# Performance work log

Hardware: AMD Instinct MI355X
Metric: run time of the kernel (lower is better)

The kernel has to match this reference:

```python
import jax, jax.numpy as jnp
import numpy as np

SL, BS, HS = 2048, 4, 1024
FFN, E, TOPK = 4096, 8, 2
T = SL * BS


def setup_inputs() -> dict:
    key = jax.random.key(0)
    k1, k2, k3, k4, k5 = jax.random.split(key, 5)
    x = jax.random.normal(k1, (SL, BS, HS), dtype=jnp.float32)
    expert_weights = jax.random.uniform(k2, (T, TOPK), dtype=jnp.float32)
    w1 = jax.random.normal(k3, (E, HS, FFN), dtype=jnp.float32) * (HS ** -0.5)
    w2 = jax.random.normal(k4, (E, FFN, HS), dtype=jnp.float32) * (FFN ** -0.5)
    expert_indices = jax.random.randint(k5, (T, TOPK), 0, E, dtype=jnp.int32)
    return {"x": x, "expert_weights": expert_weights, "w1": w1, "w2": w2,
            "expert_indices": expert_indices}


def reference(x, expert_weights, w1, w2, expert_indices):
    """Dropless MoE: dispatch each token to its top_k experts, run the
    per-expert MLP (x @ W1 -> gelu -> @ W2), combine weighted copies.

    Equivalent math to megablocks sort/gather -> grouped GEMM -> scatter:
    each (token, k) row is processed by exactly expert_indices[t, k]'s MLP
    and the results are summed back per token with expert_weights.
    """
    in_shape = x.shape
    hs = x.shape[-1]
    xf = x.reshape(-1, hs)                      # [T, H]
    top_k = expert_indices.shape[-1]
    eids = expert_indices.reshape(-1)           # [T*top_k]
    # gather: replicate each token top_k times (row j <-> token j // top_k)
    x_rep = jnp.repeat(xf, top_k, axis=0)       # [T*top_k, H]

    def per_expert(acc, ewb):
        e, w1_e, w2_e = ewb
        h = jax.nn.gelu(x_rep @ w1_e)           # [T*top_k, F]
        y = h @ w2_e                            # [T*top_k, H]
        mask = (eids == e).astype(x.dtype)[:, None]
        return acc + mask * y, None

    n_exp = w1.shape[0]
    acc0 = jnp.zeros_like(x_rep)
    out_flat, _ = jax.lax.scan(per_expert, acc0, (jnp.arange(n_exp), w1, w2))
    # scatter-combine: weighted sum of the top_k expert outputs per token
    w_flat = expert_weights.reshape(-1, 1)      # [T*top_k, 1]
    out = (w_flat * out_flat).reshape(-1, top_k, hs).sum(axis=1)
    return out.reshape(in_shape)
```

## Files before the change

### kernel.cpp

```cpp
#include <hip/hip_runtime.h>
#include <hip/hip_bf16.h>
#include <stdint.h>
#include <stddef.h>

#define SLEN 2048
#define BSZ  4
#define HSD  1024
#define FFND 4096
#define NEXP 8
#define NTOP 2
#define NTOK (SLEN*BSZ)
#define NROW (NTOK*NTOP)
#define NRP  (NROW + NEXP*128)
#define MAXT (NROW/128 + NEXP)

typedef __hip_bfloat16 bf16;
typedef __attribute__((ext_vector_type(8))) __bf16 b8v;
typedef __attribute__((ext_vector_type(4))) float f4v;

static constexpr size_t OFF_BLOCKHIST = 0;
static constexpr size_t OFF_BLOCKBASE = 2048;
static constexpr size_t OFF_SCHED_E   = 4096;
static constexpr size_t OFF_SCHED_R   = 4736;
static constexpr size_t OFF_NTILES    = 5376;
static constexpr size_t OFF_STOK      = 16384;
static constexpr size_t OFF_SWT       = OFF_STOK + 69632;
static constexpr size_t OFF_SLOT      = OFF_SWT + 69632;
static constexpr size_t OFF_XB        = 221184;
static constexpr size_t OFF_W1T       = OFF_XB  + (size_t)NTOK*HSD*2;
static constexpr size_t OFF_W2T       = OFF_W1T + (size_t)NEXP*FFND*HSD*2;
static constexpr size_t OFF_H         = OFF_W2T + (size_t)NEXP*HSD*FFND*2;
static constexpr size_t OFF_Y         = OFF_H   + (size_t)NRP*FFND*2;
static constexpr size_t WS_NEED       = OFF_Y   + (size_t)NRP*HSD*2;
static constexpr size_t OFF_YP        = OFF_XB;

__device__ __forceinline__ void gload_lds16(const void* g, void* l) {
  __builtin_amdgcn_global_load_lds(
      (const __attribute__((address_space(1))) unsigned int*)g,
      (__attribute__((address_space(3))) unsigned int*)l, 16, 0, 0);
}

__device__ __forceinline__ f4v mfma16(b8v a, b8v b, f4v c) {
  return __builtin_amdgcn_mfma_f32_16x16x32_bf16(a, b, c, 0, 0, 0);
}

__device__ __forceinline__ float gelu_tanh(float x) {
  float u = 0.7978845608028654f * x * (1.0f + 0.044715f * x * x);
  float e = __expf(2.0f * u);
  float t = 1.0f - 2.0f / (e + 1.0f);
  return 0.5f * x * (1.0f + t);
}

__global__ void moe_hist(const int* __restrict__ eidx, int* __restrict__ blockhist) {
  __shared__ int h[NEXP];
  int tid = threadIdx.x;
  if (tid < NEXP) h[tid] = 0;
  __syncthreads();
  int gid = blockIdx.x * 256 + tid;
  atomicAdd(&h[eidx[gid] & 7], 1);
  __syncthreads();
  if (tid < NEXP) blockhist[blockIdx.x * NEXP + tid] = h[tid];
}

__global__ void moe_plan(const int* __restrict__ blockhist, int* __restrict__ blockbase,
                         int* __restrict__ sched_e, int* __restrict__ sched_r,
                         int* __restrict__ ntiles,
                         int* __restrict__ stok, float* __restrict__ swt) {
  int tid = threadIdx.x;
  for (int i = tid; i < NRP; i += 256) { stok[i] = 0; swt[i] = 0.0f; }
  __syncthreads();
  if (tid == 0) {
    int cnt[NEXP], off[NEXP];
    for (int e = 0; e < NEXP; ++e) {
      int c = 0;
      for (int b = 0; b < 64; ++b) c += blockhist[b * NEXP + e];
      cnt[e] = c;
    }
    int run = 0, it = 0;
    for (int e = 0; e < NEXP; ++e) {
      off[e] = run;
      int nt = (cnt[e] + 127) >> 7;
      for (int j = 0; j < nt; ++j) { sched_e[it] = e; sched_r[it] = run + j * 128; ++it; }
      run += nt << 7;
    }
    *ntiles = it;
    for (int e = 0; e < NEXP; ++e) {
      int r = off[e];
      for (int b = 0; b < 64; ++b) { blockbase[b * NEXP + e] = r; r += blockhist[b * NEXP + e]; }
    }
  }
}

__global__ void moe_scatter(const int* __restrict__ eidx, const float* __restrict__ ew,
                            const int* __restrict__ blockbase,
                            int* __restrict__ stok, float* __restrict__ swt,
                            int* __restrict__ slot) {
  __shared__ int cur[NEXP];
  int tid = threadIdx.x;
  if (tid < NEXP) cur[tid] = blockbase[blockIdx.x * NEXP + tid];
  __syncthreads();
  int gid = blockIdx.x * 256 + tid;
  int e = eidx[gid] & 7;
  int pos = atomicAdd(&cur[e], 1);
  stok[pos] = gid >> 1;
  swt[pos]  = ew[gid];
  slot[gid] = pos;
}

__global__ void conv_x(const float* __restrict__ x, bf16* __restrict__ xb) {
  int gid = blockIdx.x * 256 + threadIdx.x;
  float4 v = ((const float4*)x)[gid];
  alignas(8) bf16 o[4];
  o[0] = __float2bfloat16(v.x); o[1] = __float2bfloat16(v.y);
  o[2] = __float2bfloat16(v.z); o[3] = __float2bfloat16(v.w);
  ((ushort4*)xb)[gid] = *(const ushort4*)o;
}

__global__ void transpose_conv(const float* __restrict__ src, bf16* __restrict__ dst,
                               int R, int C) {
  __shared__ float tile[32][65];
  int e = blockIdx.z;
  const float* s = src + (size_t)e * R * C;
  uint* d = (uint*)((ushort*)dst + (size_t)e * R * C);
  int c0 = blockIdx.x * 32, r0 = blockIdx.y * 64;
  int tx = threadIdx.x, ty = threadIdx.y;
  #pragma unroll
  for (int j = 0; j < 64; j += 8)
    tile[tx][ty + j] = s[(size_t)(r0 + ty + j) * C + (c0 + tx)];
  __syncthreads();
  #pragma unroll
  for (int j = 0; j < 32; j += 8) {
    int c = ty + j;
    alignas(4) bf16 p[2];
    p[0] = __float2bfloat16(tile[c][tx * 2]);
    p[1] = __float2bfloat16(tile[c][tx * 2 + 1]);
    d[(((size_t)(c0 + c) * R + r0) >> 1) + tx] = *(const uint*)p;
  }
}

template<int KDIM, int NDIM, int NSPLIT, bool GATHER, int ACT>
__global__ __launch_bounds__(256, 4)
void moe_gemm(const bf16* __restrict__ A, const bf16* __restrict__ B,
              bf16* __restrict__ OutBase,
              const int* __restrict__ stok,
              const int* __restrict__ sched_e, const int* __restrict__ sched_r,
              const int* __restrict__ ntiles) {
  int rt = blockIdx.y;
  if (rt >= *ntiles) return;
  const int tid  = threadIdx.x;
  const int lane = tid & 63;
  const int wid  = tid >> 6;
  const int wm = wid & 1, wn = wid >> 1;
  const int e    = sched_e[rt];
  const int row0 = sched_r[rt];
  const int n0   = blockIdx.x * 128;
  const int z    = blockIdx.z;
  const int kbase = z * (KDIM / NSPLIT);
  bf16* Out = OutBase + (size_t)z * NRP * NDIM;

  __shared__ short lds[16384];
  short* Ach = lds;
  short* Bch = lds + 8192;

  const int l15  = lane & 15;
  const int quad = lane >> 4;
  const ushort* Aus = (const ushort*)A;
  const ushort* Bexp = (const ushort*)B + (size_t)e * NDIM * KDIM;

  const int rsub  = lane >> 3;
  const int kgsrc = (lane & 7) ^ rsub;
  const ushort* aptr[4];
  const ushort* bptr[4];
  short* aLds[4];
  short* bLds[4];
  #pragma unroll
  for (int j = 0; j < 4; ++j) {
    int i  = wid * 4 + j;
    int xr = 8 * i + rsub;
    int grow = GATHER ? stok[row0 + xr] : (row0 + xr);
    aptr[j] = Aus  + (size_t)grow * KDIM + kbase + kgsrc * 8;
    bptr[j] = Bexp + (size_t)(n0 + xr) * KDIM + kbase + kgsrc * 8;
    aLds[j] = Ach + i * 512;
    bLds[j] = Bch + i * 512;
  }

  int aoff[4][2], boff[4][2];
  #pragma unroll
  for (int t = 0; t < 4; ++t) {
    int m_local = wm * 64 + t * 16 + l15;
    int n_local = wn * 64 + t * 16 + l15;
    #pragma unroll
    for (int s = 0; s < 2; ++s) {
      int kg = s * 4 + quad;
      aoff[t][s] = m_local * 64 + ((kg ^ (l15 & 7)) << 3);
      boff[t][s] = n_local * 64 + ((kg ^ (l15 & 7)) << 3);
    }
  }

  f4v acc[4][4];
  #pragma unroll
  for (int mt = 0; mt < 4; ++mt)
    #pragma unroll
    for (int nt = 0; nt < 4; ++nt) acc[mt][nt] = (f4v)0.0f;

  const int KT = KDIM / 64 / NSPLIT;
  #pragma unroll 1
  for (int kt = 0; kt < KT; ++kt) {
    __syncthreads();
    #pragma unroll
    for (int j = 0; j < 4; ++j) {
      gload_lds16(aptr[j], aLds[j]);
      gload_lds16(bptr[j], bLds[j]);
      aptr[j] += 64; bptr[j] += 64;
    }
    __syncthreads();
    #pragma unroll
    for (int s = 0; s < 2; ++s) {
      b8v af[4], bfm[4];
      #pragma unroll
      for (int mt = 0; mt < 4; ++mt)
        af[mt] = *(const b8v*)(Ach + aoff[mt][s]);
      #pragma unroll
      for (int nt = 0; nt < 4; ++nt)
        bfm[nt] = *(const b8v*)(Bch + boff[nt][s]);
      #pragma unroll
      for (int mt = 0; mt < 4; ++mt)
        #pragma unroll
        for (int nt = 0; nt < 4; ++nt)
          acc[mt][nt] = mfma16(af[mt], bfm[nt], acc[mt][nt]);
    }
  }

  #pragma unroll
  for (int mt = 0; mt < 4; ++mt)
    #pragma unroll
    for (int nt = 0; nt < 4; ++nt) {
      f4v v = acc[mt][nt];
      #pragma unroll
      for (int r = 0; r < 4; ++r) {
        int m = row0 + wm * 64 + mt * 16 + quad * 4 + r;
        int n = n0   + wn * 64 + nt * 16 + l15;
        float o = (ACT == 0) ? gelu_tanh(v[r]) : v[r];
        Out[(size_t)m * NDIM + n] = __float2bfloat16(o);
      }
    }
}

__global__ void moe_combine(const bf16* __restrict__ Yp, const float* __restrict__ swt,
                            const int* __restrict__ slot, float* __restrict__ out) {
  int gid = blockIdx.x * 256 + threadIdx.x;
  int t  = gid >> 7;
  int ho = (gid & 127) << 3;
  int s0 = slot[t * 2], s1 = slot[t * 2 + 1];
  float w0 = swt[s0], w1 = swt[s1];
  const __bf16* Y0 = (const __bf16*)Yp;
  const __bf16* Y1 = Y0 + (size_t)NRP * HSD;
  b8v a0 = *(const b8v*)(Y0 + (size_t)s0 * HSD + ho);
  b8v a1 = *(const b8v*)(Y1 + (size_t)s0 * HSD + ho);
  b8v b0 = *(const b8v*)(Y0 + (size_t)s1 * HSD + ho);
  b8v b1 = *(const b8v*)(Y1 + (size_t)s1 * HSD + ho);
  float o[8];
  #pragma unroll
  for (int i = 0; i < 8; ++i)
    o[i] = w0 * ((float)a0[i] + (float)a1[i]) + w1 * ((float)b0[i] + (float)b1[i]);
  float4* op = (float4*)(out + (size_t)t * HSD + ho);
  op[0] = make_float4(o[0], o[1], o[2], o[3]);
  op[1] = make_float4(o[4], o[5], o[6], o[7]);
}

extern "C" void kernel_launch(void* const* d_in, const int* in_sizes, int n_in,
                              void* d_out, int out_size, void* d_ws, size_t ws_size,
                              hipStream_t stream) {
  const float* x    = (const float*)d_in[0];
  const float* ew   = (const float*)d_in[1];
  const float* w1   = (const float*)d_in[2];
  const float* w2   = (const float*)d_in[3];
  const int*   eidx = (const int*)d_in[4];
  float* out = (float*)d_out;
  char* ws = (char*)d_ws;

  if (ws_size < WS_NEED) {
    hipMemsetAsync(d_out, 0x7F, 8, stream);
    return;
  }

  int*   blockhist = (int*)(ws + OFF_BLOCKHIST);
  int*   blockbase = (int*)(ws + OFF_BLOCKBASE);
  int*   sched_e   = (int*)(ws + OFF_SCHED_E);
  int*   sched_r   = (int*)(ws + OFF_SCHED_R);
  int*   ntiles    = (int*)(ws + OFF_NTILES);
  int*   stok      = (int*)(ws + OFF_STOK);
  float* swt       = (float*)(ws + OFF_SWT);
  int*   slot      = (int*)(ws + OFF_SLOT);
  bf16*  xb        = (bf16*)(ws + OFF_XB);
  bf16*  w1t       = (bf16*)(ws + OFF_W1T);
  bf16*  w2t       = (bf16*)(ws + OFF_W2T);
  bf16*  Hbuf      = (bf16*)(ws + OFF_H);
  bf16*  Ypart     = (bf16*)(ws + OFF_YP);

  moe_hist<<<64, 256, 0, stream>>>(eidx, blockhist);
  moe_plan<<<1, 256, 0, stream>>>(blockhist, blockbase, sched_e, sched_r, ntiles, stok, swt);
  moe_scatter<<<64, 256, 0, stream>>>(eidx, ew, blockbase, stok, swt, slot);

  conv_x<<<(NTOK * HSD / 4) / 256, 256, 0, stream>>>(x, xb);
  transpose_conv<<<dim3(FFND / 32, HSD / 64, NEXP), dim3(32, 8), 0, stream>>>(w1, w1t, HSD, FFND);
  transpose_conv<<<dim3(HSD / 32, FFND / 64, NEXP), dim3(32, 8), 0, stream>>>(w2, w2t, FFND, HSD);

  moe_gemm<HSD, FFND, 1, true, 0><<<dim3(FFND / 128, MAXT, 1), 256, 0, stream>>>(
      xb, w1t, Hbuf, stok, sched_e, sched_r, ntiles);
  moe_gemm<FFND, HSD, 2, false, 1><<<dim3(HSD / 128, MAXT, 2), 256, 0, stream>>>(
      Hbuf, w2t, Ypart, stok, sched_e, sched_r, ntiles);

  moe_combine<<<NTOK * HSD / 8 / 256, 256, 0, stream>>>(Ypart, swt, slot, out);
}
```

Before: 733.0 us.

## Enlarge MoE GEMM tiles to 256 rows with double-buffered LDS pipeline

Grows the grouped GEMM block tile to 256x256 for the first GEMM and 256x128 for the second, using 512-thread blocks, and pads the expert schedule to 256-row tiles. The K loop now double-buffers LDS, prefetching the next stage with direct-to-LDS loads while MFMAs run on the current one, synchronised by vmcnt waits and raw barriers, and raises wave priority during compute. The aim is more data reuse per block and hidden global load latency. In exchange, LDS use and per-wave register pressure rise, occupancy falls, and each expert carries more padding rows.

Measured after the change: 783.4 us. +6.9%, slower.

```diff
diff --git a/kernel.cpp b/kernel.cpp
--- a/kernel.cpp
+++ b/kernel.cpp
@@ -11,8 +11,8 @@
 #define NTOP 2
 #define NTOK (SLEN*BSZ)
 #define NROW (NTOK*NTOP)
-#define NRP  (NROW + NEXP*128)
-#define MAXT (NROW/128 + NEXP)
+#define NRP  (NROW + NEXP*256)
+#define MAXT (NROW/256 + NEXP)
 
 typedef __hip_bfloat16 bf16;
 typedef __attribute__((ext_vector_type(8))) __bf16 b8v;
@@ -23,15 +23,14 @@
 static constexpr size_t OFF_SCHED_E   = 4096;
 static constexpr size_t OFF_SCHED_R   = 4736;
 static constexpr size_t OFF_NTILES    = 5376;
-static constexpr size_t OFF_STOK      = 16384;
-static constexpr size_t OFF_SWT       = OFF_STOK + 69632;
-static constexpr size_t OFF_SLOT      = OFF_SWT + 69632;
+static constexpr size_t OFF_STOK      = 8192;
+static constexpr size_t OFF_SWT       = OFF_STOK + 73728;
+static constexpr size_t OFF_SLOT      = OFF_SWT + 73728;
 static constexpr size_t OFF_XB        = 221184;
 static constexpr size_t OFF_W1T       = OFF_XB  + (size_t)NTOK*HSD*2;
 static constexpr size_t OFF_W2T       = OFF_W1T + (size_t)NEXP*FFND*HSD*2;
 static constexpr size_t OFF_H         = OFF_W2T + (size_t)NEXP*HSD*FFND*2;
-static constexpr size_t OFF_Y         = OFF_H   + (size_t)NRP*FFND*2;
-static constexpr size_t WS_NEED       = OFF_Y   + (size_t)NRP*HSD*2;
+static constexpr size_t WS_NEED       = OFF_H   + (size_t)NRP*FFND*2;
 static constexpr size_t OFF_YP        = OFF_XB;
 
 __device__ __forceinline__ void gload_lds16(const void* g, void* l) {
@@ -79,9 +78,9 @@
     int run = 0, it = 0;
     for (int e = 0; e < NEXP; ++e) {
       off[e] = run;
-      int nt = (cnt[e] + 127) >> 7;
-      for (int j = 0; j < nt; ++j) { sched_e[it] = e; sched_r[it] = run + j * 128; ++it; }
-      run += nt << 7;
+      int nt = (cnt[e] + 255) >> 8;
+      for (int j = 0; j < nt; ++j) { sched_e[it] = e; sched_r[it] = run + j * 256; ++it; }
+      run += nt << 8;
     }
     *ntiles = it;
     for (int e = 0; e < NEXP; ++e) {
@@ -138,29 +137,38 @@
   }
 }
 
-template<int KDIM, int NDIM, int NSPLIT, bool GATHER, int ACT>
-__global__ __launch_bounds__(256, 4)
+template<int KDIM, int NDIM, int BN, int NSPLIT, bool GATHER, int ACT>
+__global__ __launch_bounds__(512, 2)
 void moe_gemm(const bf16* __restrict__ A, const bf16* __restrict__ B,
               bf16* __restrict__ OutBase,
               const int* __restrict__ stok,
               const int* __restrict__ sched_e, const int* __restrict__ sched_r,
               const int* __restrict__ ntiles) {
+  constexpr int BM = 256, BK = 64;
+  constexpr int WN = BN / 64;
+  constexpr int WM = 8 / WN;
+  constexpr int WTM = BM / WM;
+  constexpr int MF = WTM / 16;
+  constexpr int NF = 4;
+  constexpr int A_LOADS = (BM * BK) / (512 * 8);
+  constexpr int B_LOADS = (BN * BK) / (512 * 8);
+  constexpr int TLOADS  = A_LOADS + B_LOADS;
+  constexpr int BUFS = (BM + BN) * BK;
+
   int rt = blockIdx.y;
   if (rt >= *ntiles) return;
   const int tid  = threadIdx.x;
   const int lane = tid & 63;
   const int wid  = tid >> 6;
-  const int wm = wid & 1, wn = wid >> 1;
+  const int wm = wid % WM, wn = wid / WM;
   const int e    = sched_e[rt];
   const int row0 = sched_r[rt];
-  const int n0   = blockIdx.x * 128;
+  const int n0   = blockIdx.x * BN;
   const int z    = blockIdx.z;
   const int kbase = z * (KDIM / NSPLIT);
   bf16* Out = OutBase + (size_t)z * NRP * NDIM;
 
-  __shared__ short lds[16384];
-  short* Ach = lds;
-  short* Bch = lds + 8192;
+  __shared__ short lds[2 * BUFS];
 
   const int l15  = lane & 15;
   const int quad = lane >> 4;
@@ -169,76 +177,106 @@
 
   const int rsub  = lane >> 3;
   const int kgsrc = (lane & 7) ^ rsub;
-  const ushort* aptr[4];
-  const ushort* bptr[4];
-  short* aLds[4];
-  short* bLds[4];
-  #pragma unroll
-  for (int j = 0; j < 4; ++j) {
-    int i  = wid * 4 + j;
+  const ushort* aptr[A_LOADS];
+  const ushort* bptr[B_LOADS];
+  #pragma unroll
+  for (int j = 0; j < A_LOADS; ++j) {
+    int i  = wid * A_LOADS + j;
     int xr = 8 * i + rsub;
     int grow = GATHER ? stok[row0 + xr] : (row0 + xr);
     aptr[j] = Aus  + (size_t)grow * KDIM + kbase + kgsrc * 8;
+  }
+  #pragma unroll
+  for (int j = 0; j < B_LOADS; ++j) {
+    int i  = wid * B_LOADS + j;
+    int xr = 8 * i + rsub;
     bptr[j] = Bexp + (size_t)(n0 + xr) * KDIM + kbase + kgsrc * 8;
-    aLds[j] = Ach + i * 512;
-    bLds[j] = Bch + i * 512;
-  }
-
-  int aoff[4][2], boff[4][2];
-  #pragma unroll
-  for (int t = 0; t < 4; ++t) {
-    int m_local = wm * 64 + t * 16 + l15;
-    int n_local = wn * 64 + t * 16 + l15;
+  }
+
+  int aoff[MF][2], boff[NF][2];
+  #pragma unroll
+  for (int t = 0; t < MF; ++t) {
+    int m_local = wm * WTM + t * 16 + l15;
     #pragma unroll
     for (int s = 0; s < 2; ++s) {
       int kg = s * 4 + quad;
       aoff[t][s] = m_local * 64 + ((kg ^ (l15 & 7)) << 3);
+    }
+  }
+  #pragma unroll
+  for (int t = 0; t < NF; ++t) {
+    int n_local = wn * 64 + t * 16 + l15;
+    #pragma unroll
+    for (int s = 0; s < 2; ++s) {
+      int kg = s * 4 + quad;
       boff[t][s] = n_local * 64 + ((kg ^ (l15 & 7)) << 3);
     }
   }
 
-  f4v acc[4][4];
-  #pragma unroll
-  for (int mt = 0; mt < 4; ++mt)
-    #pragma unroll
-    for (int nt = 0; nt < 4; ++nt) acc[mt][nt] = (f4v)0.0f;
-
-  const int KT = KDIM / 64 / NSPLIT;
-  #pragma unroll 1
+  f4v acc[MF][NF];
+  #pragma unroll
+  for (int mt = 0; mt < MF; ++mt)
+    #pragma unroll
+    for (int nt = 0; nt < NF; ++nt) acc[mt][nt] = (f4v)0.0f;
+
+  auto STAGE = [&](int par) {
+    short* ab = lds + par * BUFS;
+    short* bb = ab + BM * BK;
+    #pragma unroll
+    for (int j = 0; j < A_LOADS; ++j) {
+      gload_lds16(aptr[j], ab + (wid * A_LOADS + j) * 512);
+      aptr[j] += BK;
+    }
+    #pragma unroll
+    for (int j = 0; j < B_LOADS; ++j) {
+      gload_lds16(bptr[j], bb + (wid * B_LOADS + j) * 512);
+      bptr[j] += BK;
+    }
+  };
+
+  STAGE(0);
+  const int KT = KDIM / BK / NSPLIT;
+  #pragma unroll 2
   for (int kt = 0; kt < KT; ++kt) {
-    __syncthreads();
-    #pragma unroll
-    for (int j = 0; j < 4; ++j) {
-      gload_lds16(aptr[j], aLds[j]);
-      gload_lds16(bptr[j], bLds[j]);
-      aptr[j] += 64; bptr[j] += 64;
-    }
-    __syncthreads();
+    asm volatile("" ::: "memory");
+    __builtin_amdgcn_s_barrier();
+    if (kt + 1 < KT) {
+      STAGE((kt + 1) & 1);
+      if constexpr (TLOADS == 8) asm volatile("s_waitcnt vmcnt(8)" ::: "memory");
+      else                       asm volatile("s_waitcnt vmcnt(6)" ::: "memory");
+    } else {
+      asm volatile("s_waitcnt vmcnt(0)" ::: "memory");
+    }
+    __builtin_amdgcn_s_barrier();
+    const short* Ab = lds + (kt & 1) * BUFS;
+    const short* Bb = Ab + BM * BK;
+    __builtin_amdgcn_s_setprio(1);
     #pragma unroll
     for (int s = 0; s < 2; ++s) {
-      b8v af[4], bfm[4];
+      b8v af[MF], bfm[NF];
       #pragma unroll
-      for (int mt = 0; mt < 4; ++mt)
-        af[mt] = *(const b8v*)(Ach + aoff[mt][s]);
+      for (int mt = 0; mt < MF; ++mt)
+        af[mt] = *(const b8v*)(Ab + aoff[mt][s]);
       #pragma unroll
-      for (int nt = 0; nt < 4; ++nt)
-        bfm[nt] = *(const b8v*)(Bch + boff[nt][s]);
+      for (int nt = 0; nt < NF; ++nt)
+        bfm[nt] = *(const b8v*)(Bb + boff[nt][s]);
       #pragma unroll
-      for (int mt = 0; mt < 4; ++mt)
+      for (int mt = 0; mt < MF; ++mt)
         #pragma unroll
-        for (int nt = 0; nt < 4; ++nt)
+        for (int nt = 0; nt < NF; ++nt)
           acc[mt][nt] = mfma16(af[mt], bfm[nt], acc[mt][nt]);
     }
-  }
-
-  #pragma unroll
-  for (int mt = 0; mt < 4; ++mt)
-    #pragma unroll
-    for (int nt = 0; nt < 4; ++nt) {
+    __builtin_amdgcn_s_setprio(0);
+  }
+
+  #pragma unroll
+  for (int mt = 0; mt < MF; ++mt)
+    #pragma unroll
+    for (int nt = 0; nt < NF; ++nt) {
       f4v v = acc[mt][nt];
       #pragma unroll
       for (int r = 0; r < 4; ++r) {
-        int m = row0 + wm * 64 + mt * 16 + quad * 4 + r;
+        int m = row0 + wm * WTM + mt * 16 + quad * 4 + r;
         int n = n0   + wn * 64 + nt * 16 + l15;
         float o = (ACT == 0) ? gelu_tanh(v[r]) : v[r];
         Out[(size_t)m * NDIM + n] = __float2bfloat16(o);
@@ -306,9 +344,9 @@
   transpose_conv<<<dim3(FFND / 32, HSD / 64, NEXP), dim3(32, 8), 0, stream>>>(w1, w1t, HSD, FFND);
   transpose_conv<<<dim3(HSD / 32, FFND / 64, NEXP), dim3(32, 8), 0, stream>>>(w2, w2t, FFND, HSD);
 
-  moe_gemm<HSD, FFND, 1, true, 0><<<dim3(FFND / 128, MAXT, 1), 256, 0, stream>>>(
+  moe_gemm<HSD, FFND, 256, 1, true, 0><<<dim3(FFND / 256, MAXT, 1), 512, 0, stream>>>(
       xb, w1t, Hbuf, stok, sched_e, sched_r, ntiles);
-  moe_gemm<FFND, HSD, 2, false, 1><<<dim3(HSD / 128, MAXT, 2), 256, 0, stream>>>(
+  moe_gemm<FFND, HSD, 128, 2, false, 1><<<dim3(HSD / 128, MAXT, 2), 512, 0, stream>>>(
       Hbuf, w2t, Ypart, stok, sched_e, sched_r, ntiles);
 
   moe_combine<<<NTOK * HSD / 8 / 256, 256, 0, stream>>>(Ypart, swt, slot, out);
```

## Use 256x256 double-buffered GEMM tiles with interleaved prefetch in MoE kernels

Applied to the files above, without the earlier changes.

The grouped GEMM moves from 128x128 tiles with 256 threads to 256x256 tiles with 512 threads. LDS is double-buffered and the K loop is software-pipelined, so global-to-LDS loads for the next K step are issued between quarter-tile MFMA phases, with explicit waitcnt, barriers and setprio. Expert row padding grows to 256, and the unused Y buffer is removed from the workspace. This aims to raise arithmetic intensity and hide load latency, at the cost of more padded rows, fewer blocks (lower occupancy) and higher register pressure from the 8x4 accumulator array.

New measurement: 734.7 us. About the same (+0.2%).

```diff
diff --git a/kernel.cpp b/kernel.cpp
--- a/kernel.cpp
+++ b/kernel.cpp
@@ -11,8 +11,8 @@
 #define NTOP 2
 #define NTOK (SLEN*BSZ)
 #define NROW (NTOK*NTOP)
-#define NRP  (NROW + NEXP*128)
-#define MAXT (NROW/128 + NEXP)
+#define NRP  (NROW + NEXP*256)
+#define MAXT (NROW/256 + NEXP)
 
 typedef __hip_bfloat16 bf16;
 typedef __attribute__((ext_vector_type(8))) __bf16 b8v;
@@ -23,15 +23,14 @@
 static constexpr size_t OFF_SCHED_E   = 4096;
 static constexpr size_t OFF_SCHED_R   = 4736;
 static constexpr size_t OFF_NTILES    = 5376;
-static constexpr size_t OFF_STOK      = 16384;
-static constexpr size_t OFF_SWT       = OFF_STOK + 69632;
-static constexpr size_t OFF_SLOT      = OFF_SWT + 69632;
+static constexpr size_t OFF_STOK      = 8192;
+static constexpr size_t OFF_SWT       = OFF_STOK + 73728;
+static constexpr size_t OFF_SLOT      = OFF_SWT + 73728;
 static constexpr size_t OFF_XB        = 221184;
 static constexpr size_t OFF_W1T       = OFF_XB  + (size_t)NTOK*HSD*2;
 static constexpr size_t OFF_W2T       = OFF_W1T + (size_t)NEXP*FFND*HSD*2;
 static constexpr size_t OFF_H         = OFF_W2T + (size_t)NEXP*HSD*FFND*2;
-static constexpr size_t OFF_Y         = OFF_H   + (size_t)NRP*FFND*2;
-static constexpr size_t WS_NEED       = OFF_Y   + (size_t)NRP*HSD*2;
+static constexpr size_t WS_NEED       = OFF_H   + (size_t)NRP*FFND*2;
 static constexpr size_t OFF_YP        = OFF_XB;
 
 __device__ __forceinline__ void gload_lds16(const void* g, void* l) {
@@ -79,9 +78,9 @@
     int run = 0, it = 0;
     for (int e = 0; e < NEXP; ++e) {
       off[e] = run;
-      int nt = (cnt[e] + 127) >> 7;
-      for (int j = 0; j < nt; ++j) { sched_e[it] = e; sched_r[it] = run + j * 128; ++it; }
-      run += nt << 7;
+      int nt = (cnt[e] + 255) >> 8;
+      for (int j = 0; j < nt; ++j) { sched_e[it] = e; sched_r[it] = run + j * 256; ++it; }
+      run += nt << 8;
     }
     *ntiles = it;
     for (int e = 0; e < NEXP; ++e) {
@@ -139,12 +138,17 @@
 }
 
 template<int KDIM, int NDIM, int NSPLIT, bool GATHER, int ACT>
-__global__ __launch_bounds__(256, 4)
+__global__ __launch_bounds__(512, 2)
 void moe_gemm(const bf16* __restrict__ A, const bf16* __restrict__ B,
               bf16* __restrict__ OutBase,
               const int* __restrict__ stok,
               const int* __restrict__ sched_e, const int* __restrict__ sched_r,
               const int* __restrict__ ntiles) {
+  constexpr int BM = 256, BN = 256, BK = 64;
+  constexpr int BUFS = (BM + BN) * BK;
+  constexpr int KT = KDIM / BK / NSPLIT;
+  constexpr int JT = KT / 2;
+
   int rt = blockIdx.y;
   if (rt >= *ntiles) return;
   const int tid  = threadIdx.x;
@@ -153,93 +157,138 @@
   const int wm = wid & 1, wn = wid >> 1;
   const int e    = sched_e[rt];
   const int row0 = sched_r[rt];
-  const int n0   = blockIdx.x * 128;
+  const int n0   = blockIdx.x * BN;
   const int z    = blockIdx.z;
   const int kbase = z * (KDIM / NSPLIT);
   bf16* Out = OutBase + (size_t)z * NRP * NDIM;
 
-  __shared__ short lds[16384];
-  short* Ach = lds;
-  short* Bch = lds + 8192;
+  __shared__ short lds[2 * BUFS];
 
   const int l15  = lane & 15;
   const int quad = lane >> 4;
-  const ushort* Aus = (const ushort*)A;
+  const int xor7 = l15 & 7;
+  const ushort* Aus  = (const ushort*)A;
   const ushort* Bexp = (const ushort*)B + (size_t)e * NDIM * KDIM;
 
   const int rsub  = lane >> 3;
   const int kgsrc = (lane & 7) ^ rsub;
-  const ushort* aptr[4];
-  const ushort* bptr[4];
-  short* aLds[4];
-  short* bLds[4];
-  #pragma unroll
-  for (int j = 0; j < 4; ++j) {
-    int i  = wid * 4 + j;
-    int xr = 8 * i + rsub;
-    int grow = GATHER ? stok[row0 + xr] : (row0 + xr);
-    aptr[j] = Aus  + (size_t)grow * KDIM + kbase + kgsrc * 8;
-    bptr[j] = Bexp + (size_t)(n0 + xr) * KDIM + kbase + kgsrc * 8;
-    aLds[j] = Ach + i * 512;
-    bLds[j] = Bch + i * 512;
+  const ushort* aP[2][2];
+  const ushort* bP[2][2];
+  #pragma unroll
+  for (int h = 0; h < 2; ++h)
+    #pragma unroll
+    for (int q = 0; q < 2; ++q) {
+      int xr = 128 * h + 8 * (2 * wid + q) + rsub;
+      int grow = GATHER ? stok[row0 + xr] : (row0 + xr);
+      aP[h][q] = Aus  + (size_t)grow * KDIM + kbase + kgsrc * 8;
+      bP[h][q] = Bexp + (size_t)(n0 + xr) * KDIM + kbase + kgsrc * 8;
+    }
+
+  auto SA = [&](int b, int h, int T) {
+    #pragma unroll
+    for (int q = 0; q < 2; ++q)
+      gload_lds16(aP[h][q] + T * 64, lds + b * BUFS + h * 8192 + (2 * wid + q) * 512);
+  };
+  auto SB = [&](int b, int h, int T) {
+    #pragma unroll
+    for (int q = 0; q < 2; ++q)
+      gload_lds16(bP[h][q] + T * 64, lds + b * BUFS + BM * BK + h * 8192 + (2 * wid + q) * 512);
+  };
+
+  const int goff0 = (quad ^ xor7) << 3;
+  const int goff1 = ((4 + quad) ^ xor7) << 3;
+  const int mbase = (wm * 128 + l15) * 64;
+  const int nbase = BM * BK + (wn * 64 + l15) * 64;
+
+  f4v acc[8][4];
+  #pragma unroll
+  for (int mt = 0; mt < 8; ++mt)
+    #pragma unroll
+    for (int nt = 0; nt < 4; ++nt) acc[mt][nt] = (f4v)0.0f;
+
+  b8v aF[2][4], bF0[2][2], bF1[2][2];
+
+  auto LDA = [&](int b, int qm) {
+    const short* base = lds + b * BUFS + mbase + qm * 4096;
+    #pragma unroll
+    for (int t = 0; t < 4; ++t) {
+      aF[0][t] = *(const b8v*)(base + t * 1024 + goff0);
+      aF[1][t] = *(const b8v*)(base + t * 1024 + goff1);
+    }
+  };
+  auto LDB = [&](int b, int qn, b8v (&bF)[2][2]) {
+    const short* base = lds + b * BUFS + nbase + qn * 2048;
+    #pragma unroll
+    for (int u = 0; u < 2; ++u) {
+      bF[0][u] = *(const b8v*)(base + u * 1024 + goff0);
+      bF[1][u] = *(const b8v*)(base + u * 1024 + goff1);
+    }
+  };
+  auto MM = [&](int qm, int qn, b8v (&bF)[2][2]) {
+    __builtin_amdgcn_s_setprio(1);
+    #pragma unroll
+    for (int s = 0; s < 2; ++s)
+      #pragma unroll
+      for (int t = 0; t < 4; ++t)
+        #pragma unroll
+        for (int u = 0; u < 2; ++u)
+          acc[qm * 4 + t][qn * 2 + u] = mfma16(aF[s][t], bF[s][u], acc[qm * 4 + t][qn * 2 + u]);
+    __builtin_amdgcn_s_setprio(0);
+  };
+  auto BAR = [&] {
+    asm volatile("" ::: "memory");
+    __builtin_amdgcn_s_barrier();
+    asm volatile("" ::: "memory");
+  };
+
+  SB(0, 0, 0); SB(0, 1, 0); SA(0, 0, 0); SA(0, 1, 0);
+  SB(1, 0, 1); SB(1, 1, 1);
+  asm volatile("s_waitcnt vmcnt(4)" ::: "memory");
+  __builtin_amdgcn_s_barrier();
+  asm volatile("" ::: "memory");
+
+  #pragma unroll 1
+  for (int j = 0; j < JT; ++j) {
+    const int t1 = 2 * j + 1, t2 = 2 * j + 2, t3 = 2 * j + 3;
+    const bool more = (j + 1 < JT);
+    LDA(0, 0); LDB(0, 0, bF0);
+    SA(1, 0, t1);
+    BAR(); MM(0, 0, bF0); BAR();
+    LDB(0, 1, bF1);
+    SA(1, 1, t1);
+    BAR(); MM(0, 1, bF1); BAR();
+    LDA(0, 1);
+    if (more) SB(0, 0, t2);
+    BAR(); MM(1, 1, bF1); BAR();
+    if (more) SB(0, 1, t2);
+    BAR(); MM(1, 0, bF0);
+    if (more) asm volatile("s_waitcnt vmcnt(4)" ::: "memory");
+    else      asm volatile("s_waitcnt vmcnt(0)" ::: "memory");
+    BAR();
+    LDA(1, 0); LDB(1, 0, bF0);
+    if (more) SA(0, 0, t2);
+    BAR(); MM(0, 0, bF0); BAR();
+    LDB(1, 1, bF1);
+    if (more) SA(0, 1, t2);
+    BAR(); MM(0, 1, bF1); BAR();
+    LDA(1, 1);
+    if (more) SB(1, 0, t3);
+    BAR(); MM(1, 1, bF1); BAR();
+    if (more) SB(1, 1, t3);
+    BAR(); MM(1, 0, bF0);
+    asm volatile("s_waitcnt vmcnt(4)" ::: "memory");
+    BAR();
   }
 
-  int aoff[4][2], boff[4][2];
-  #pragma unroll
-  for (int t = 0; t < 4; ++t) {
-    int m_local = wm * 64 + t * 16 + l15;
-    int n_local = wn * 64 + t * 16 + l15;
-    #pragma unroll
-    for (int s = 0; s < 2; ++s) {
-      int kg = s * 4 + quad;
-      aoff[t][s] = m_local * 64 + ((kg ^ (l15 & 7)) << 3);
-      boff[t][s] = n_local * 64 + ((kg ^ (l15 & 7)) << 3);
-    }
-  }
-
-  f4v acc[4][4];
-  #pragma unroll
-  for (int mt = 0; mt < 4; ++mt)
-    #pragma unroll
-    for (int nt = 0; nt < 4; ++nt) acc[mt][nt] = (f4v)0.0f;
-
-  const int KT = KDIM / 64 / NSPLIT;
-  #pragma unroll 1
-  for (int kt = 0; kt < KT; ++kt) {
-    __syncthreads();
-    #pragma unroll
-    for (int j = 0; j < 4; ++j) {
-      gload_lds16(aptr[j], aLds[j]);
-      gload_lds16(bptr[j], bLds[j]);
-      aptr[j] += 64; bptr[j] += 64;
-    }
-    __syncthreads();
-    #pragma unroll
-    for (int s = 0; s < 2; ++s) {
-      b8v af[4], bfm[4];
-      #pragma unroll
-      for (int mt = 0; mt < 4; ++mt)
-        af[mt] = *(const b8v*)(Ach + aoff[mt][s]);
-      #pragma unroll
-      for (int nt = 0; nt < 4; ++nt)
-        bfm[nt] = *(const b8v*)(Bch + boff[nt][s]);
-      #pragma unroll
-      for (int mt = 0; mt < 4; ++mt)
-        #pragma unroll
-        for (int nt = 0; nt < 4; ++nt)
-          acc[mt][nt] = mfma16(af[mt], bfm[nt], acc[mt][nt]);
-    }
-  }
-
-  #pragma unroll
-  for (int mt = 0; mt < 4; ++mt)
+  #pragma unroll
+  for (int mt = 0; mt < 8; ++mt)
     #pragma unroll
     for (int nt = 0; nt < 4; ++nt) {
       f4v v = acc[mt][nt];
       #pragma unroll
       for (int r = 0; r < 4; ++r) {
-        int m = row0 + wm * 64 + mt * 16 + quad * 4 + r;
-        int n = n0   + wn * 64 + nt * 16 + l15;
+        int m = row0 + wm * 128 + mt * 16 + quad * 4 + r;
+        int n = n0   + wn * 64  + nt * 16 + l15;
         float o = (ACT == 0) ? gelu_tanh(v[r]) : v[r];
         Out[(size_t)m * NDIM + n] = __float2bfloat16(o);
       }
@@ -306,9 +355,9 @@
   transpose_conv<<<dim3(FFND / 32, HSD / 64, NEXP), dim3(32, 8), 0, stream>>>(w1, w1t, HSD, FFND);
   transpose_conv<<<dim3(HSD / 32, FFND / 64, NEXP), dim3(32, 8), 0, stream>>>(w2, w2t, FFND, HSD);
 
-  moe_gemm<HSD, FFND, 1, true, 0><<<dim3(FFND / 128, MAXT, 1), 256, 0, stream>>>(
+  moe_gemm<HSD, FFND, 1, true, 0><<<dim3(FFND / 256, MAXT, 1), 512, 0, stream>>>(
       xb, w1t, Hbuf, stok, sched_e, sched_r, ntiles);
-  moe_gemm<FFND, HSD, 2, false, 1><<<dim3(HSD / 128, MAXT, 2), 256, 0, stream>>>(
+  moe_gemm<FFND, HSD, 2, false, 1><<<dim3(HSD / 256, MAXT, 2), 512, 0, stream>>>(
       Hbuf, w2t, Ypart, stok, sched_e, sched_r, ntiles);
 
   moe_combine<<<NTOK * HSD / 8 / 256, 256, 0, stream>>>(Ypart, swt, slot, out);
```
